# Optimization experiments

Measured on AMD Instinct MI355X. Metric: run time of the kernel, lower is better.

## Reference

```python
import jax, jax.numpy as jnp
import numpy as np

H_RES, W_RES = 32, 32
DIM = 512
NUM_HEADS = 16
HEAD_DIM = DIM // NUM_HEADS
SCALE = HEAD_DIM ** -0.5
B = 16
N = H_RES * W_RES
TABLE_SIZE = (2 * H_RES - 1) * (2 * W_RES - 1)


def _relative_position_index():
    coords_h = np.arange(H_RES)
    coords_w = np.arange(W_RES)
    coords = np.stack(np.meshgrid(coords_h, coords_w, indexing='ij'))  # [2, H, W]
    coords_flat = coords.reshape(2, -1)  # [2, N]
    rel = coords_flat[:, :, None] - coords_flat[:, None, :]  # [2, N, N]
    rel = rel.transpose(1, 2, 0).astype(np.int64)  # [N, N, 2]
    rel[:, :, 0] += H_RES - 1
    rel[:, :, 1] += W_RES - 1
    rel[:, :, 0] *= 2 * W_RES - 1
    return rel.sum(-1)  # [N, N]


def setup_inputs() -> dict:
    key = jax.random.key(0)
    ks = jax.random.split(key, 6)
    x = jax.random.normal(ks[0], (B, N, DIM), dtype=jnp.float32)
    w_qkv = jax.random.normal(ks[1], (DIM, 3 * DIM), dtype=jnp.float32) * (DIM ** -0.5)
    b_qkv = jnp.zeros((3 * DIM,), dtype=jnp.float32)
    w_proj = jax.random.normal(ks[2], (DIM, DIM), dtype=jnp.float32) * (DIM ** -0.5)
    b_proj = jnp.zeros((DIM,), dtype=jnp.float32)
    bias_table = jax.random.normal(ks[3], (TABLE_SIZE, NUM_HEADS), dtype=jnp.float32) * 0.02
    rel_index = jnp.asarray(_relative_position_index(), dtype=jnp.int32)
    return {"x": x, "w_qkv": w_qkv, "b_qkv": b_qkv, "w_proj": w_proj,
            "b_proj": b_proj, "bias_table": bias_table, "rel_index": rel_index}


def reference(x, w_qkv, b_qkv, w_proj, b_proj, bias_table, rel_index):
    Bq, Nq, C = x.shape
    qkv = x @ w_qkv + b_qkv  # [B, N, 3C]
    qkv = qkv.reshape(Bq, Nq, 3, NUM_HEADS, HEAD_DIM)
    q = qkv[:, :, 0].transpose(0, 2, 1, 3) * SCALE  # [B, nH, N, d]
    k = qkv[:, :, 1].transpose(0, 2, 1, 3)
    v = qkv[:, :, 2].transpose(0, 2, 1, 3)
    attn = jnp.einsum('bhnd,bhmd->bhnm', q, k)  # [B, nH, N, N]
    bias = bias_table[rel_index]  # [N, N, nH]
    attn = attn + bias.transpose(2, 0, 1)[None]  # broadcast over batch
    attn = jax.nn.softmax(attn, axis=-1)
    out = jnp.einsum('bhnm,bhmd->bhnd', attn, v)  # [B, nH, N, d]
    out = out.transpose(0, 2, 1, 3).reshape(Bq, Nq, C)
    return out @ w_proj + b_proj
```

## Files before the change

### kernel.cpp

```cpp
#include <hip/hip_runtime.h>
#include <hip/hip_bf16.h>
#include <cstdint>
#include <cstddef>

typedef _Float16 f16;
typedef __attribute__((ext_vector_type(8))) _Float16 f16x8;
typedef __attribute__((ext_vector_type(4))) _Float16 f16x4v;
typedef __bf16 bf16;
typedef __attribute__((ext_vector_type(4))) float f32x4;
typedef __attribute__((ext_vector_type(16))) float f32x16;

#define LOG2E 1.4426950408889634f
#define QK_SCALE 0.17677669529663687f

__device__ __forceinline__ f32x4 mfma16f(f16x8 a, f16x8 b, f32x4 c) {
  return __builtin_amdgcn_mfma_f32_16x16x32_f16(a, b, c, 0, 0, 0);
}
__device__ __forceinline__ f32x16 mfma32f(f16x8 a, f16x8 b, f32x16 c) {
  return __builtin_amdgcn_mfma_f32_32x32x16_f16(a, b, c, 0, 0, 0);
}
__device__ __forceinline__ float exp2_hw(float x) {
  float r; asm("v_exp_f32 %0, %1" : "=v"(r) : "v"(x)); return r;
}
__device__ __forceinline__ uint32_t cvtpk_f16(float a, float b) {
  uint32_t r; asm("v_cvt_pkrtz_f16_f32 %0, %1, %2" : "=v"(r) : "v"(a), "v"(b)); return r;
}
__device__ __forceinline__ float lo16f(uint32_t u) { return __uint_as_float(u << 16); }
__device__ __forceinline__ float hi16f(uint32_t u) { return __uint_as_float(u & 0xFFFF0000u); }

__device__ __forceinline__ void gl16(const f16* g, f16* l) {
  __builtin_amdgcn_global_load_lds(
      (const __attribute__((address_space(1))) void*)g,
      (__attribute__((address_space(3))) void*)l, 16, 0, 0);
}

__device__ __forceinline__ uint32_t packoff(int m, int k) {
  return (((uint32_t)(m >> 7) * 16u + (uint32_t)(k >> 5)) * 8u + (uint32_t)((m >> 4) & 7)) * 512u
       + (uint32_t)((k >> 3) & 3) * 128u + (uint32_t)(m & 15) * 8u + (uint32_t)(k & 7);
}

__global__ __launch_bounds__(256) void prep_kernel(
    const float* __restrict__ x, const float* __restrict__ wqkv, const float* __restrict__ wproj,
    f16* __restrict__ Xp, f16* __restrict__ Wq, f16* __restrict__ Wp)
{
  const int X4 = 16384 * 512 / 4;
  int e = blockIdx.x * 256 + threadIdx.x;
  if (e < X4) {
    int m = e >> 7, k4 = e & 127;
    f32x4 v = *(const f32x4*)(x + (size_t)e * 4);
    f16x4v o;
    #pragma unroll
    for (int j = 0; j < 4; ++j) o[j] = (f16)v[j];
    *(f16x4v*)(Xp + packoff(m, k4 * 4)) = o;
  } else if (e < X4 + 1536 * 512) {
    int e2 = e - X4;
    int n = e2 >> 9, k = e2 & 511;
    Wq[packoff(n, k)] = (f16)wqkv[k * 1536 + n];
  } else {
    int e3 = e - (X4 + 1536 * 512);
    if (e3 < 512 * 512) {
      int n = e3 >> 9, k = e3 & 511;
      Wp[packoff(n, k)] = (f16)wproj[k * 512 + n];
    }
  }
}

__global__ __launch_bounds__(256) void tblT_kernel(
    const float* __restrict__ btab, float* __restrict__ tblT)
{
  int e = blockIdx.x * 256 + threadIdx.x;
  if (e < 3969 * 16) {
    int h = e & 15, i = e >> 4;
    tblT[h * 4000 + i] = btab[e] * LOG2E;
  }
}

__global__ __launch_bounds__(256) void biasC_kernel(
    const float* __restrict__ tblT, bf16* __restrict__ biasC)
{
  int t = blockIdx.x * 256 + threadIdx.x;
  if (t >= 16 * 63 * 64) return;
  int lane = t & 63;
  int sh = t >> 6;
  int s = sh % 63, h = sh / 63;
  int lq = lane & 31, hi5 = lane >> 5;
  const float* row = tblT + h * 4000 + s * 63 + 31 + lq;
  bf16 o[16];
  #pragma unroll
  for (int r = 0; r < 16; ++r) {
    int kx = (r & 3) + 8 * (r >> 2) + 4 * hi5;
    o[r] = (bf16)row[-kx];
  }
  *(uint4*)(biasC + (size_t)t * 16) = *(uint4*)&o[0];
  *(uint4*)(biasC + (size_t)t * 16 + 8) = *(uint4*)&o[8];
}

template<int NB>
__global__ __launch_bounds__(256) void gemm_frag(
    const f16* __restrict__ Ap, const f16* __restrict__ Bp,
    const float* __restrict__ bvec,
    f16* __restrict__ Qp, f16* __restrict__ Kp, f16* __restrict__ Vt,
    float* __restrict__ out)
{
  __shared__ f16 sA[3][4096];
  __shared__ f16 sB[3][4096];
  const int bid = blockIdx.x;
  const int xcd = bid & 7, idx = bid >> 3;
  int mb, nb;
  if (NB == 12) { int q = idx / 12; mb = xcd * 16 + q; nb = idx - q * 12; }
  else          { mb = xcd * 16 + (idx >> 2); nb = idx & 3; }
  const int tid = threadIdx.x, lane = tid & 63, wave = tid >> 6;
  const int l15 = lane & 15, l4 = lane >> 4;
  const int wr = wave >> 1, wc = wave & 1;

  const f16* gA = Ap + (uint32_t)mb * 65536u + (uint32_t)wave * 1024u + (uint32_t)lane * 8u;
  const f16* gB = Bp + (uint32_t)nb * 65536u + (uint32_t)wave * 1024u + (uint32_t)lane * 8u;
  const int wl = wave * 1024;

  gl16(gA,        &sA[0][wl]);
  gl16(gA + 512,  &sA[0][wl + 512]);
  gl16(gB,        &sB[0][wl]);
  gl16(gB + 512,  &sB[0][wl + 512]);
  gl16(gA + 4096, &sA[1][wl]);
  gl16(gA + 4608, &sA[1][wl + 512]);
  gl16(gB + 4096, &sB[1][wl]);
  gl16(gB + 4608, &sB[1][wl + 512]);

  f32x4 acc[4][4];
  #pragma unroll
  for (int i = 0; i < 4; ++i)
    #pragma unroll
    for (int j = 0; j < 4; ++j) acc[i][j] = (f32x4){0.f, 0.f, 0.f, 0.f};

  const uint32_t aoff = (uint32_t)(wr * 4) * 512u + (uint32_t)lane * 8u;
  const uint32_t boff = (uint32_t)(wc * 4) * 512u + (uint32_t)lane * 8u;

  #pragma unroll
  for (int kt = 0; kt < 16; ++kt) {
    const int s2 = (kt + 2) % 3;
    gl16(gA + (kt + 2) * 4096,       &sA[s2][wl]);
    gl16(gA + (kt + 2) * 4096 + 512, &sA[s2][wl + 512]);
    gl16(gB + (kt + 2) * 4096,       &sB[s2][wl]);
    gl16(gB + (kt + 2) * 4096 + 512, &sB[s2][wl + 512]);
    asm volatile("s_waitcnt vmcnt(8)" ::: "memory");
    asm volatile("s_barrier" ::: "memory");
    const int s0 = kt % 3;
    f16x8 af[4], bfr[4];
    #pragma unroll
    for (int f = 0; f < 4; ++f) {
      af[f]  = *(const f16x8*)&sA[s0][aoff + f * 512];
      bfr[f] = *(const f16x8*)&sB[s0][boff + f * 512];
    }
    asm volatile("s_waitcnt lgkmcnt(0)" ::: "memory");
    asm volatile("s_barrier" ::: "memory");
    #pragma unroll
    for (int mf = 0; mf < 4; ++mf)
      #pragma unroll
      for (int nf = 0; nf < 4; ++nf)
        acc[mf][nf] = mfma16f(af[mf], bfr[nf], acc[mf][nf]);
  }
  asm volatile("s_waitcnt vmcnt(0)" ::: "memory");

  #pragma unroll
  for (int mf = 0; mf < 4; ++mf) {
    #pragma unroll
    for (int nf = 0; nf < 4; ++nf) {
      int colb = nb * 128 + wc * 64 + nf * 16 + l15;
      float bb = bvec[colb];
      #pragma unroll
      for (int i = 0; i < 4; ++i) {
        int m = mb * 128 + wr * 64 + mf * 16 + l4 * 4 + i;
        float v = acc[mf][nf][i] + bb;
        if (NB == 4) {
          out[(size_t)m * 512 + colb] = v;
        } else {
          int t = colb >> 9, cc = colb & 511;
          int b = m >> 10, n = m & 1023;
          int hh = cc >> 5, d = cc & 31;
          int bh2 = b * 16 + hh;
          if (t == 0) {
            v *= (QK_SCALE * LOG2E);
            uint32_t off = (((uint32_t)bh2 * 32u + (uint32_t)(n >> 5)) * 2u + (uint32_t)(d >> 4)) * 512u
                         + ((uint32_t)((d >> 3) & 1) * 32u + (uint32_t)(n & 31)) * 8u + (uint32_t)(d & 7);
            Qp[off] = (f16)v;
          } else if (t == 1) {
            Kp[((size_t)(bh2 * 2 + (d >> 4)) * 1024 + n) * 16 + (d & 15)] = (f16)v;
          } else {
            int nl = n & 15;
            int npl = (nl >= 4 && nl < 12) ? (nl ^ 12) : nl;
            int np = (n & ~15) | npl;
            Vt[((size_t)(bh2 * 128 + (np >> 3)) * 32 + d) * 8 + (np & 7)] = (f16)v;
          }
        }
      }
    }
  }
}

__global__ __launch_bounds__(256) void attn_kernel(
    const f16* __restrict__ Qp, const f16* __restrict__ Kp, const f16* __restrict__ Vt,
    const bf16* __restrict__ biasC, f16* __restrict__ Op)
{
  const int bid = blockIdx.x;
  const int xcd = bid & 7, slot = bid >> 3;
  const int h = xcd * 2 + (slot >> 6);
  const int rest = slot & 63;
  const int qg = rest >> 4, b = rest & 15;
  const int bh = b * 16 + h;
  const int tid = threadIdx.x, lane = tid & 63, wave = tid >> 6;
  const int lq = lane & 31, hi5 = lane >> 5;

  const int qb0 = qg * 8 + wave * 2;
  const int m0 = b * 1024 + qb0 * 32;

  const uint32_t qbase = ((uint32_t)bh * 32u + (uint32_t)qb0) * 1024u + (uint32_t)lane * 8u;
  const f16x8 q00 = *(const f16x8*)(Qp + qbase);
  const f16x8 q01 = *(const f16x8*)(Qp + qbase + 512);
  const f16x8 q10 = *(const f16x8*)(Qp + qbase + 1024);
  const f16x8 q11 = *(const f16x8*)(Qp + qbase + 1536);

  uint32_t koff = (uint32_t)bh * 32768u + (uint32_t)lq * 16u + (uint32_t)hi5 * 8u;
  uint32_t voff = (uint32_t)bh * 32768u + (uint32_t)hi5 * 256u + (uint32_t)lq * 8u;
  const bf16* bp = biasC + ((uint32_t)(h * 63 + qb0 + 31) * 64u + (uint32_t)lane) * 16u;

  f16x8 kA0 = *(const f16x8*)(Kp + koff);
  f16x8 kA1 = *(const f16x8*)(Kp + koff + 16384);
  uint4 p0A = *(const uint4*)(bp);
  uint4 p1A = *(const uint4*)(bp + 8);
  uint4 p2A = *(const uint4*)(bp + 1024);
  uint4 p3A = *(const uint4*)(bp + 1032);
  f16x8 vA0 = *(const f16x8*)(Vt + voff);
  f16x8 vA1 = *(const f16x8*)(Vt + voff + 512);
  f16x8 kB0 = *(const f16x8*)(Kp + koff + 512);
  f16x8 kB1 = *(const f16x8*)(Kp + koff + 16384 + 512);
  uint4 p0B = *(const uint4*)(bp - 1024);
  uint4 p1B = *(const uint4*)(bp - 1016);
  uint4 p2B = *(const uint4*)(bp);
  uint4 p3B = *(const uint4*)(bp + 8);
  f16x8 vB0 = *(const f16x8*)(Vt + voff + 1024);
  f16x8 vB1 = *(const f16x8*)(Vt + voff + 1536);

  f32x16 O0, O1;
  #pragma unroll
  for (int i = 0; i < 16; ++i) { O0[i] = 0.f; O1[i] = 0.f; }
  f32x4 racc0 = {0.f, 0.f, 0.f, 0.f}, racc1 = {0.f, 0.f, 0.f, 0.f};

  union Uf { uint32_t u[4]; f16x8 v; };

#define UNPACK16(S, Pa, Pb)                              \
  S[0]  = lo16f(Pa.x); S[1]  = hi16f(Pa.x);              \
  S[2]  = lo16f(Pa.y); S[3]  = hi16f(Pa.y);              \
  S[4]  = lo16f(Pa.z); S[5]  = hi16f(Pa.z);              \
  S[6]  = lo16f(Pa.w); S[7]  = hi16f(Pa.w);              \
  S[8]  = lo16f(Pb.x); S[9]  = hi16f(Pb.x);              \
  S[10] = lo16f(Pb.y); S[11] = hi16f(Pb.y);              \
  S[12] = lo16f(Pb.z); S[13] = hi16f(Pb.z);              \
  S[14] = lo16f(Pb.w); S[15] = hi16f(Pb.w);

  auto tile = [&](f16x8& K0, f16x8& K1, f16x8& V0, f16x8& V1,
                  uint4& P0, uint4& P1, uint4& P2, uint4& P3,
                  uint32_t kpre, uint32_t vpre, int bpre) {
    asm volatile("s_waitcnt vmcnt(8)" ::: "memory");
    f32x16 S0, S1;
    UNPACK16(S0, P0, P1)
    UNPACK16(S1, P2, P3)
    S0 = mfma32f(K0, q00, S0);
    S0 = mfma32f(K1, q01, S0);
    S1 = mfma32f(K0, q10, S1);
    S1 = mfma32f(K1, q11, S1);
    K0 = *(const f16x8*)(Kp + koff + kpre);
    K1 = *(const f16x8*)(Kp + koff + 16384 + kpre);
    P0 = *(const uint4*)(bp + bpre);
    P1 = *(const uint4*)(bp + bpre + 8);
    P2 = *(const uint4*)(bp + bpre + 1024);
    P3 = *(const uint4*)(bp + bpre + 1032);
    __builtin_amdgcn_sched_barrier(0);
    {
      float e0  = exp2_hw(S0[0]),  e1  = exp2_hw(S0[1]),  e2  = exp2_hw(S0[2]),  e3  = exp2_hw(S0[3]);
      float e4  = exp2_hw(S0[4]),  e5  = exp2_hw(S0[5]),  e6  = exp2_hw(S0[6]),  e7  = exp2_hw(S0[7]);
      float e8  = exp2_hw(S0[8]),  e9  = exp2_hw(S0[9]),  e10 = exp2_hw(S0[10]), e11 = exp2_hw(S0[11]);
      float e12 = exp2_hw(S0[12]), e13 = exp2_hw(S0[13]), e14 = exp2_hw(S0[14]), e15 = exp2_hw(S0[15]);
      racc0[0] += e0 + e4;   racc0[1] += e1 + e5;
      racc0[2] += e2 + e6;   racc0[3] += e3 + e7;
      racc0[0] += e8 + e12;  racc0[1] += e9 + e13;
      racc0[2] += e10 + e14; racc0[3] += e11 + e15;
      Uf a1, a2;
      a1.u[0] = cvtpk_f16(e0,  e1);  a1.u[1] = cvtpk_f16(e2,  e3);
      a1.u[2] = cvtpk_f16(e4,  e5);  a1.u[3] = cvtpk_f16(e6,  e7);
      a2.u[0] = cvtpk_f16(e8,  e9);  a2.u[1] = cvtpk_f16(e10, e11);
      a2.u[2] = cvtpk_f16(e12, e13); a2.u[3] = cvtpk_f16(e14, e15);
      O0 = mfma32f(a1.v, V0, O0);
      O0 = mfma32f(a2.v, V1, O0);
    }
    {
      float e0  = exp2_hw(S1[0]),  e1  = exp2_hw(S1[1]),  e2  = exp2_hw(S1[2]),  e3  = exp2_hw(S1[3]);
      float e4  = exp2_hw(S1[4]),  e5  = exp2_hw(S1[5]),  e6  = exp2_hw(S1[6]),  e7  = exp2_hw(S1[7]);
      float e8  = exp2_hw(S1[8]),  e9  = exp2_hw(S1[9]),  e10 = exp2_hw(S1[10]), e11 = exp2_hw(S1[11]);
      float e12 = exp2_hw(S1[12]), e13 = exp2_hw(S1[13]), e14 = exp2_hw(S1[14]), e15 = exp2_hw(S1[15]);
      racc1[0] += e0 + e4;   racc1[1] += e1 + e5;
      racc1[2] += e2 + e6;   racc1[3] += e3 + e7;
      racc1[0] += e8 + e12;  racc1[1] += e9 + e13;
      racc1[2] += e10 + e14; racc1[3] += e11 + e15;
      Uf a1, a2;
      a1.u[0] = cvtpk_f16(e0,  e1);  a1.u[1] = cvtpk_f16(e2,  e3);
      a1.u[2] = cvtpk_f16(e4,  e5);  a1.u[3] = cvtpk_f16(e6,  e7);
      a2.u[0] = cvtpk_f16(e8,  e9);  a2.u[1] = cvtpk_f16(e10, e11);
      a2.u[2] = cvtpk_f16(e12, e13); a2.u[3] = cvtpk_f16(e14, e15);
      O1 = mfma32f(a1.v, V0, O1);
      O1 = mfma32f(a2.v, V1, O1);
    }
    V0 = *(const f16x8*)(Vt + voff + vpre);
    V1 = *(const f16x8*)(Vt + voff + vpre + 512);
    __builtin_amdgcn_sched_barrier(0);
  };

  #pragma unroll 1
  for (int it = 0; it < 16; ++it) {
    tile(kA0, kA1, vA0, vA1, p0A, p1A, p2A, p3A, 1024u, 2048u, -2048);
    tile(kB0, kB1, vB0, vB1, p0B, p1B, p2B, p3B, 1536u, 3072u, -3072);
    koff += 1024u; voff += 2048u; bp -= 2048;
  }

  float rs0 = (racc0[0] + racc0[1]) + (racc0[2] + racc0[3]);
  rs0 += __shfl_xor(rs0, 32);
  float inv0 = 1.0f / rs0;
  float rs1 = (racc1[0] + racc1[1]) + (racc1[2] + racc1[3]);
  rs1 += __shfl_xor(rs1, 32);
  float inv1 = 1.0f / rs1;

  const int kcol = h * 32 + lq;
  #pragma unroll
  for (int r = 0; r < 16; ++r) {
    int qrow = (r & 3) + 8 * (r >> 2) + 4 * hi5;
    float t0 = __shfl(inv0, qrow);
    float t1 = __shfl(inv1, qrow);
    Op[packoff(m0 + qrow, kcol)] = (f16)(O0[r] * t0);
    Op[packoff(m0 + 32 + qrow, kcol)] = (f16)(O1[r] * t1);
  }
}

extern "C" void kernel_launch(void* const* d_in, const int* in_sizes, int n_in,
                              void* d_out, int out_size, void* d_ws, size_t ws_size,
                              hipStream_t stream) {
  const float* x     = (const float*)d_in[0];
  const float* wqkv  = (const float*)d_in[1];
  const float* bqkv  = (const float*)d_in[2];
  const float* wproj = (const float*)d_in[3];
  const float* bproj = (const float*)d_in[4];
  const float* btab  = (const float*)d_in[5];
  float* out = (float*)d_out;

  char* ws = (char*)d_ws;
  size_t off = 0;
  auto walloc = [&](size_t bytes) {
    void* p = ws + off;
    off += (bytes + 255) & ~(size_t)255;
    return p;
  };
  const size_t PAD = 262144;
  f16* Xp   = (f16*)walloc((size_t)16384 * 512 * 2 + PAD);
  f16* Wq   = (f16*)walloc((size_t)1536 * 512 * 2 + PAD);
  f16* Wp   = (f16*)walloc((size_t)512 * 512 * 2 + PAD);
  float* tblT = (float*)walloc((size_t)16 * 4000 * 4);
  f16* Qp   = (f16*)walloc((size_t)16384 * 512 * 2 + PAD);
  f16* Kp   = (f16*)walloc((size_t)16384 * 512 * 2 + PAD);
  f16* Vt   = (f16*)walloc((size_t)16384 * 512 * 2 + PAD);
  bf16* biasC = (bf16*)walloc((size_t)16 * 63 * 64 * 16 * 2 + PAD);
  f16* Op   = (f16*)walloc((size_t)16384 * 512 * 2 + PAD);

  const int prep_total = 16384 * 512 / 4 + 1536 * 512 + 512 * 512;
  prep_kernel<<<(prep_total + 255) / 256, 256, 0, stream>>>(
      x, wqkv, wproj, Xp, Wq, Wp);

  tblT_kernel<<<(3969 * 16 + 255) / 256, 256, 0, stream>>>(btab, tblT);

  biasC_kernel<<<(16 * 63 * 64 + 255) / 256, 256, 0, stream>>>(tblT, biasC);

  gemm_frag<12><<<1536, 256, 0, stream>>>(
      Xp, Wq, bqkv, Qp, Kp, Vt, nullptr);

  attn_kernel<<<1024, 256, 0, stream>>>(Qp, Kp, Vt, biasC, Op);

  gemm_frag<4><<<512, 256, 0, stream>>>(
      Op, Wp, bproj, nullptr, nullptr, nullptr, out);
}
```

Measured before the change: 160.7 us.

## Vectorize prep packing, drop a GEMM barrier, sum softmax rows with fdot2

The prep kernel now has each thread produce 16 contiguous f16 elements of the packed fragment layout. It reads x with wide loads and writes 16-byte stores, instead of scattered 8-byte or 2-byte writes. The GEMM main loop waits for the current stage, reads LDS, then issues the prefetch for stage kt+2, which removes the second barrier and the lgkmcnt wait per k-step. In attention, row sums are accumulated with fdot2 on the already-packed f16 exponentials rather than separate f32 adds. This cuts VALU work, but the sums are now built from f16-rounded values.

```diff
diff --git a/kernel.cpp b/kernel.cpp
--- a/kernel.cpp
+++ b/kernel.cpp
@@ -5,7 +5,7 @@
 
 typedef _Float16 f16;
 typedef __attribute__((ext_vector_type(8))) _Float16 f16x8;
-typedef __attribute__((ext_vector_type(4))) _Float16 f16x4v;
+typedef __attribute__((ext_vector_type(2))) _Float16 f16x2;
 typedef __bf16 bf16;
 typedef __attribute__((ext_vector_type(4))) float f32x4;
 typedef __attribute__((ext_vector_type(16))) float f32x16;
@@ -27,6 +27,12 @@
 }
 __device__ __forceinline__ float lo16f(uint32_t u) { return __uint_as_float(u << 16); }
 __device__ __forceinline__ float hi16f(uint32_t u) { return __uint_as_float(u & 0xFFFF0000u); }
+
+__device__ __forceinline__ float dot2acc(uint32_t u, float acc) {
+  union { uint32_t x; f16x2 h; } c; c.x = u;
+  f16x2 one2 = {(_Float16)1.0f, (_Float16)1.0f};
+  return __builtin_amdgcn_fdot2(c.h, one2, acc, false);
+}
 
 __device__ __forceinline__ void gl16(const f16* g, f16* l) {
   __builtin_amdgcn_global_load_lds(
@@ -43,25 +49,59 @@
     const float* __restrict__ x, const float* __restrict__ wqkv, const float* __restrict__ wproj,
     f16* __restrict__ Xp, f16* __restrict__ Wq, f16* __restrict__ Wp)
 {
-  const int X4 = 16384 * 512 / 4;
-  int e = blockIdx.x * 256 + threadIdx.x;
-  if (e < X4) {
-    int m = e >> 7, k4 = e & 127;
-    f32x4 v = *(const f32x4*)(x + (size_t)e * 4);
-    f16x4v o;
-    #pragma unroll
-    for (int j = 0; j < 4; ++j) o[j] = (f16)v[j];
-    *(f16x4v*)(Xp + packoff(m, k4 * 4)) = o;
-  } else if (e < X4 + 1536 * 512) {
-    int e2 = e - X4;
-    int n = e2 >> 9, k = e2 & 511;
-    Wq[packoff(n, k)] = (f16)wqkv[k * 1536 + n];
+  const int XT  = 16384 * 512 / 16;
+  const int WQT = 1536 * 512 / 16;
+  int t = blockIdx.x * 256 + threadIdx.x;
+  if (t < XT) {
+    uint32_t o = (uint32_t)t * 16u;
+    uint32_t blk = o >> 9, rem = o & 511u;
+    uint32_t k23 = rem >> 7, r16 = (rem >> 3) & 15u;
+    uint32_t i7 = blk & 7u, k5 = (blk >> 3) & 15u, m7 = blk >> 7;
+    uint32_t m = m7 * 128u + i7 * 16u + r16;
+    uint32_t k = k5 * 32u + k23 * 8u;
+    const float* s0 = x + (size_t)m * 512 + k;
+    f32x4 a0 = *(const f32x4*)s0;
+    f32x4 a1 = *(const f32x4*)(s0 + 4);
+    f32x4 b0 = *(const f32x4*)(s0 + 512);
+    f32x4 b1 = *(const f32x4*)(s0 + 516);
+    f16 ov[16];
+    #pragma unroll
+    for (int j = 0; j < 4; ++j) {
+      ov[j] = (f16)a0[j]; ov[4 + j] = (f16)a1[j];
+      ov[8 + j] = (f16)b0[j]; ov[12 + j] = (f16)b1[j];
+    }
+    *(uint4*)(Xp + o) = *(uint4*)&ov[0];
+    *(uint4*)(Xp + o + 8) = *(uint4*)&ov[8];
+  } else if (t < XT + WQT) {
+    uint32_t o = (uint32_t)(t - XT) * 16u;
+    uint32_t blk = o >> 9, rem = o & 511u;
+    uint32_t k23 = rem >> 7, r16 = (rem >> 3) & 15u;
+    uint32_t i7 = blk & 7u, k5 = (blk >> 3) & 15u, m7 = blk >> 7;
+    uint32_t n = m7 * 128u + i7 * 16u + r16;
+    uint32_t k = k5 * 32u + k23 * 8u;
+    f16 ov[16];
+    #pragma unroll
+    for (int j = 0; j < 8; ++j) {
+      ov[j] = (f16)wqkv[(size_t)(k + j) * 1536 + n];
+      ov[8 + j] = (f16)wqkv[(size_t)(k + j) * 1536 + n + 1];
+    }
+    *(uint4*)(Wq + o) = *(uint4*)&ov[0];
+    *(uint4*)(Wq + o + 8) = *(uint4*)&ov[8];
   } else {
-    int e3 = e - (X4 + 1536 * 512);
-    if (e3 < 512 * 512) {
-      int n = e3 >> 9, k = e3 & 511;
-      Wp[packoff(n, k)] = (f16)wproj[k * 512 + n];
-    }
+    uint32_t o = (uint32_t)(t - XT - WQT) * 16u;
+    uint32_t blk = o >> 9, rem = o & 511u;
+    uint32_t k23 = rem >> 7, r16 = (rem >> 3) & 15u;
+    uint32_t i7 = blk & 7u, k5 = (blk >> 3) & 15u, m7 = blk >> 7;
+    uint32_t n = m7 * 128u + i7 * 16u + r16;
+    uint32_t k = k5 * 32u + k23 * 8u;
+    f16 ov[16];
+    #pragma unroll
+    for (int j = 0; j < 8; ++j) {
+      ov[j] = (f16)wproj[(size_t)(k + j) * 512 + n];
+      ov[8 + j] = (f16)wproj[(size_t)(k + j) * 512 + n + 1];
+    }
+    *(uint4*)(Wp + o) = *(uint4*)&ov[0];
+    *(uint4*)(Wp + o + 8) = *(uint4*)&ov[8];
   }
 }
 
@@ -137,22 +177,20 @@
 
   #pragma unroll
   for (int kt = 0; kt < 16; ++kt) {
+    asm volatile("s_waitcnt vmcnt(4)" ::: "memory");
+    asm volatile("s_barrier" ::: "memory");
+    const int s0 = kt % 3;
+    f16x8 af[4], bfr[4];
+    #pragma unroll
+    for (int f = 0; f < 4; ++f) {
+      af[f]  = *(const f16x8*)&sA[s0][aoff + f * 512];
+      bfr[f] = *(const f16x8*)&sB[s0][boff + f * 512];
+    }
     const int s2 = (kt + 2) % 3;
     gl16(gA + (kt + 2) * 4096,       &sA[s2][wl]);
     gl16(gA + (kt + 2) * 4096 + 512, &sA[s2][wl + 512]);
     gl16(gB + (kt + 2) * 4096,       &sB[s2][wl]);
     gl16(gB + (kt + 2) * 4096 + 512, &sB[s2][wl + 512]);
-    asm volatile("s_waitcnt vmcnt(8)" ::: "memory");
-    asm volatile("s_barrier" ::: "memory");
-    const int s0 = kt % 3;
-    f16x8 af[4], bfr[4];
-    #pragma unroll
-    for (int f = 0; f < 4; ++f) {
-      af[f]  = *(const f16x8*)&sA[s0][aoff + f * 512];
-      bfr[f] = *(const f16x8*)&sB[s0][boff + f * 512];
-    }
-    asm volatile("s_waitcnt lgkmcnt(0)" ::: "memory");
-    asm volatile("s_barrier" ::: "memory");
     #pragma unroll
     for (int mf = 0; mf < 4; ++mf)
       #pragma unroll
@@ -280,15 +318,15 @@
       float e4  = exp2_hw(S0[4]),  e5  = exp2_hw(S0[5]),  e6  = exp2_hw(S0[6]),  e7  = exp2_hw(S0[7]);
       float e8  = exp2_hw(S0[8]),  e9  = exp2_hw(S0[9]),  e10 = exp2_hw(S0[10]), e11 = exp2_hw(S0[11]);
       float e12 = exp2_hw(S0[12]), e13 = exp2_hw(S0[13]), e14 = exp2_hw(S0[14]), e15 = exp2_hw(S0[15]);
-      racc0[0] += e0 + e4;   racc0[1] += e1 + e5;
-      racc0[2] += e2 + e6;   racc0[3] += e3 + e7;
-      racc0[0] += e8 + e12;  racc0[1] += e9 + e13;
-      racc0[2] += e10 + e14; racc0[3] += e11 + e15;
       Uf a1, a2;
       a1.u[0] = cvtpk_f16(e0,  e1);  a1.u[1] = cvtpk_f16(e2,  e3);
       a1.u[2] = cvtpk_f16(e4,  e5);  a1.u[3] = cvtpk_f16(e6,  e7);
       a2.u[0] = cvtpk_f16(e8,  e9);  a2.u[1] = cvtpk_f16(e10, e11);
       a2.u[2] = cvtpk_f16(e12, e13); a2.u[3] = cvtpk_f16(e14, e15);
+      racc0[0] = dot2acc(a1.u[0], racc0[0]); racc0[1] = dot2acc(a1.u[1], racc0[1]);
+      racc0[2] = dot2acc(a1.u[2], racc0[2]); racc0[3] = dot2acc(a1.u[3], racc0[3]);
+      racc0[0] = dot2acc(a2.u[0], racc0[0]); racc0[1] = dot2acc(a2.u[1], racc0[1]);
+      racc0[2] = dot2acc(a2.u[2], racc0[2]); racc0[3] = dot2acc(a2.u[3], racc0[3]);
       O0 = mfma32f(a1.v, V0, O0);
       O0 = mfma32f(a2.v, V1, O0);
     }
@@ -297,15 +335,15 @@
       float e4  = exp2_hw(S1[4]),  e5  = exp2_hw(S1[5]),  e6  = exp2_hw(S1[6]),  e7  = exp2_hw(S1[7]);
       float e8  = exp2_hw(S1[8]),  e9  = exp2_hw(S1[9]),  e10 = exp2_hw(S1[10]), e11 = exp2_hw(S1[11]);
       float e12 = exp2_hw(S1[12]), e13 = exp2_hw(S1[13]), e14 = exp2_hw(S1[14]), e15 = exp2_hw(S1[15]);
-      racc1[0] += e0 + e4;   racc1[1] += e1 + e5;
-      racc1[2] += e2 + e6;   racc1[3] += e3 + e7;
-      racc1[0] += e8 + e12;  racc1[1] += e9 + e13;
-      racc1[2] += e10 + e14; racc1[3] += e11 + e15;
       Uf a1, a2;
       a1.u[0] = cvtpk_f16(e0,  e1);  a1.u[1] = cvtpk_f16(e2,  e3);
       a1.u[2] = cvtpk_f16(e4,  e5);  a1.u[3] = cvtpk_f16(e6,  e7);
       a2.u[0] = cvtpk_f16(e8,  e9);  a2.u[1] = cvtpk_f16(e10, e11);
       a2.u[2] = cvtpk_f16(e12, e13); a2.u[3] = cvtpk_f16(e14, e15);
+      racc1[0] = dot2acc(a1.u[0], racc1[0]); racc1[1] = dot2acc(a1.u[1], racc1[1]);
+      racc1[2] = dot2acc(a1.u[2], racc1[2]); racc1[3] = dot2acc(a1.u[3], racc1[3]);
+      racc1[0] = dot2acc(a2.u[0], racc1[0]); racc1[1] = dot2acc(a2.u[1], racc1[1]);
+      racc1[2] = dot2acc(a2.u[2], racc1[2]); racc1[3] = dot2acc(a2.u[3], racc1[3]);
       O1 = mfma32f(a1.v, V0, O1);
       O1 = mfma32f(a2.v, V1, O1);
     }
@@ -368,9 +406,8 @@
   bf16* biasC = (bf16*)walloc((size_t)16 * 63 * 64 * 16 * 2 + PAD);
   f16* Op   = (f16*)walloc((size_t)16384 * 512 * 2 + PAD);
 
-  const int prep_total = 16384 * 512 / 4 + 1536 * 512 + 512 * 512;
-  prep_kernel<<<(prep_total + 255) / 256, 256, 0, stream>>>(
-      x, wqkv, wproj, Xp, Wq, Wp);
+  const int prep_blocks = (16384 * 512 / 16 + 1536 * 512 / 16 + 512 * 512 / 16) / 256;
+  prep_kernel<<<prep_blocks, 256, 0, stream>>>(x, wqkv, wproj, Xp, Wq, Wp);
 
   tblT_kernel<<<(3969 * 16 + 255) / 256, 256, 0, stream>>>(btab, tblT);
 
```

Measured after the change: 159.9 us. About the same (-0.5%).
